# Kernel optimization log

Hardware: AMD Instinct MI355X
Metric: run time of the kernel (lower is better)

The kernel has to match this reference:

```python
import jax, jax.numpy as jnp
import numpy as np

N_EXPERTS = 6
TOP_K = 2
IN_DIM, HID_DIM, OUT_DIM = 1024, 4096, 1024
N_TOKENS = 8192


def setup_inputs() -> dict:
    key = jax.random.key(0)
    ks = jax.random.split(key, 7)
    s_in = 1.0 / np.sqrt(IN_DIM)
    s_hid = 1.0 / np.sqrt(HID_DIM)
    return {
        "x": jax.random.normal(ks[0], (N_TOKENS, IN_DIM), dtype=jnp.float32),
        "Wg": jax.random.uniform(ks[1], (IN_DIM, N_EXPERTS), jnp.float32, -s_in, s_in),
        "bg": jax.random.uniform(ks[2], (N_EXPERTS,), jnp.float32, -s_in, s_in),
        "W1": jax.random.uniform(ks[3], (N_EXPERTS, IN_DIM, HID_DIM), jnp.float32, -s_in, s_in),
        "b1": jax.random.uniform(ks[4], (N_EXPERTS, HID_DIM), jnp.float32, -s_in, s_in),
        "W2": jax.random.uniform(ks[5], (N_EXPERTS, HID_DIM, OUT_DIM), jnp.float32, -s_hid, s_hid),
        "b2": jax.random.uniform(ks[6], (N_EXPERTS, OUT_DIM), jnp.float32, -s_hid, s_hid),
    }


def reference(x, Wg, bg, W1, b1, W2, b2):
    n_experts = Wg.shape[-1]
    # gating: scores [N, E]
    scores = x @ Wg + bg
    _, topk_idx = jax.lax.top_k(scores, TOP_K)  # [N, k]
    # binary mask of selected experts [N, E]
    mask = jax.nn.one_hot(topk_idx, n_experts, dtype=scores.dtype).sum(axis=1)
    weights = jax.nn.softmax(scores, axis=-1) * mask
    weights = weights / (weights.sum(axis=-1, keepdims=True) + 1e-8)
    # dense all-expert compute (faithful to original): hidden [N, E, H]
    h = jax.nn.relu(jnp.einsum("ni,eih->neh", x, W1) + b1)
    outputs = jnp.einsum("neh,eho->neo", h, W2) + b2  # [N, E, O]
    return jnp.einsum("ne,neo->no", weights, outputs)
```

## Files before the change

### kernel.cpp

```cpp
#include <hip/hip_runtime.h>

typedef unsigned short u16;
typedef float f32x4 __attribute__((ext_vector_type(4)));
typedef __bf16 bf16x8 __attribute__((ext_vector_type(8)));
typedef unsigned short u16x8 __attribute__((ext_vector_type(8)));
typedef unsigned short u16x4 __attribute__((ext_vector_type(4)));

#define N_TOKENS 8192
#define IN_DIM   1024
#define HID_DIM  4096
#define OUT_DIM  1024
#define N_EXP    6

__device__ __forceinline__ u16 f2bf(float f) {
  union { float f; unsigned int u; } v; v.f = f;
  unsigned int u = v.u;
  unsigned int r = (u + 0x7FFFu + ((u >> 16) & 1u)) >> 16;
  return (u16)r;
}

__device__ __forceinline__ float bf2f(u16 v) {
  union { unsigned int u; float f; } x; x.u = ((unsigned int)v) << 16; return x.f;
}

__device__ __forceinline__ void load_lds16(const void* g, void* l) {
  __builtin_amdgcn_global_load_lds(
      (const __attribute__((address_space(1))) void*)g,
      (__attribute__((address_space(3))) void*)l, 16, 0, 0);
}

__global__ __launch_bounds__(256) void cvt_kernel(const float* __restrict__ src,
                                                  u16* __restrict__ dst, int n4) {
  int gid = blockIdx.x * 256 + threadIdx.x;
  int stride = gridDim.x * 256;
  for (int i = gid; i < n4; i += stride) {
    float4 v = ((const float4*)src)[i];
    u16x4 o; o[0] = f2bf(v.x); o[1] = f2bf(v.y); o[2] = f2bf(v.z); o[3] = f2bf(v.w);
    ((u16x4*)dst)[i] = o;
  }
}

__global__ __launch_bounds__(256) void transpose_cvt(const float* __restrict__ src,
                                                     u16* __restrict__ dst, int R, int C) {
  __shared__ u16 tile[64][72];
  const size_t esz = (size_t)R * C;
  src += (size_t)blockIdx.z * esz;
  dst += (size_t)blockIdx.z * esz;
  int c0 = blockIdx.x * 64, r0 = blockIdx.y * 64;
  int t = threadIdx.x;
  int cc = (t & 15) * 4, rb = t >> 4;
#pragma unroll
  for (int p = 0; p < 4; p++) {
    int r = p * 16 + rb;
    float4 v = *(const float4*)(src + (size_t)(r0 + r) * C + c0 + cc);
    tile[cc + 0][r] = f2bf(v.x);
    tile[cc + 1][r] = f2bf(v.y);
    tile[cc + 2][r] = f2bf(v.z);
    tile[cc + 3][r] = f2bf(v.w);
  }
  __syncthreads();
  int c = t >> 2, rp = (t & 3) * 16;
  u16* dp = dst + (size_t)(c0 + c) * R + r0 + rp;
  *(u16x8*)(dp)     = *(const u16x8*)&tile[c][rp];
  *(u16x8*)(dp + 8) = *(const u16x8*)&tile[c][rp + 8];
}

__global__ __launch_bounds__(256) void gating_kernel(const float* __restrict__ x,
                                                     const float* __restrict__ Wg,
                                                     const float* __restrict__ bg,
                                                     int* __restrict__ gate_e,
                                                     float* __restrict__ gate_w) {
  int lane = threadIdx.x & 63, wid = threadIdx.x >> 6;
  int tok = blockIdx.x * 4 + wid;
  float acc[N_EXP] = {0.f, 0.f, 0.f, 0.f, 0.f, 0.f};
  const float4* xr = (const float4*)(x + (size_t)tok * IN_DIM);
#pragma unroll
  for (int g = 0; g < 4; g++) {
    float4 v = xr[lane + g * 64];
    int c0 = (lane + g * 64) * 4;
#pragma unroll
    for (int c = 0; c < 4; c++) {
      float xv = (c == 0) ? v.x : (c == 1) ? v.y : (c == 2) ? v.z : v.w;
      const float* wr = Wg + (c0 + c) * N_EXP;
#pragma unroll
      for (int e = 0; e < N_EXP; e++) acc[e] += xv * wr[e];
    }
  }
#pragma unroll
  for (int e = 0; e < N_EXP; e++) {
    float a = acc[e];
#pragma unroll
    for (int off = 32; off > 0; off >>= 1) a += __shfl_xor(a, off, 64);
    acc[e] = a;
  }
  if (lane == 0) {
    float s[N_EXP];
#pragma unroll
    for (int e = 0; e < N_EXP; e++) s[e] = acc[e] + bg[e];
    float mx = s[0];
#pragma unroll
    for (int e = 1; e < N_EXP; e++) mx = fmaxf(mx, s[e]);
    float p[N_EXP], sum = 0.f;
#pragma unroll
    for (int e = 0; e < N_EXP; e++) { p[e] = expf(s[e] - mx); sum += p[e]; }
    int a = 0;
#pragma unroll
    for (int e = 1; e < N_EXP; e++) if (s[e] > s[a]) a = e;
    int b = (a == 0) ? 1 : 0;
#pragma unroll
    for (int e = 0; e < N_EXP; e++) if (e != a && s[e] > s[b]) b = e;
    float pa = p[a] / sum, pb = p[b] / sum;
    float den = pa + pb + 1e-8f;
    gate_e[2 * tok] = a; gate_e[2 * tok + 1] = b;
    gate_w[2 * tok] = pa / den; gate_w[2 * tok + 1] = pb / den;
  }
}

__global__ __launch_bounds__(384) void routing_kernel(const int* __restrict__ gate_e,
                                                      const float* __restrict__ gate_w,
                                                      int* __restrict__ idxl,
                                                      int* __restrict__ tokslot,
                                                      int* __restrict__ meta) {
  int wave = threadIdx.x >> 6, lane = threadIdx.x & 63;
  __shared__ int s_cnt[N_EXP];
  if (wave < N_EXP) {
    int e = wave, cnt = 0;
    for (int base = 0; base < N_TOKENS; base += 64) {
      int t = base + lane;
      int e0 = gate_e[2 * t], e1 = gate_e[2 * t + 1];
      bool sel = (e0 == e) || (e1 == e);
      unsigned long long m = __ballot(sel);
      int pos = __popcll(m & ((1ull << lane) - 1ull));
      if (sel) {
        int j = cnt + pos;
        idxl[e * N_TOKENS + j] = t;
        int k = (e0 == e) ? 0 : 1;
        tokslot[2 * t + k] = j;
      }
      cnt += __popcll(m);
    }
    if (lane == 0) s_cnt[e] = cnt;
  }
  __syncthreads();
  if (threadIdx.x == 0) {
    int off = 0;
    for (int e = 0; e < N_EXP; e++) { meta[e] = s_cnt[e]; meta[8 + e] = off; off += s_cnt[e]; }
    meta[8 + N_EXP] = off;
  }
}


#define GDS_A(AH) \
  _Pragma("unroll") for (int mi = 0; mi < 4; mi++) { \
    int r_ = (AH)*128 + wr*64 + mi*16 + lrow; \
    af[mi][0] = *(const bf16x8*)&sA[cur][r_*64 + ((lhi ^ lx7) * 8)]; \
    af[mi][1] = *(const bf16x8*)&sA[cur][r_*64 + (((4 + lhi) ^ lx7) * 8)]; }

#define GDS_B(BH) \
  _Pragma("unroll") for (int nj = 0; nj < 2; nj++) { \
    int r_ = (BH)*128 + wc*32 + nj*16 + lrow; \
    bfr[nj][0] = *(const bf16x8*)&sB[cur][r_*64 + ((lhi ^ lx7) * 8)]; \
    bfr[nj][1] = *(const bf16x8*)&sB[cur][r_*64 + (((4 + lhi) ^ lx7) * 8)]; }

#define GSTG_A(HH) \
  load_lds16(pa[HH][0] + ksn, &sA[nxt][((HH)*128 + wave*16) * 64]); \
  load_lds16(pa[HH][1] + ksn, &sA[nxt][((HH)*128 + wave*16 + 8) * 64]);

#define GSTG_B(HH) \
  load_lds16(pb[HH][0] + ksn, &sB[nxt][((HH)*128 + wave*16) * 64]); \
  load_lds16(pb[HH][1] + ksn, &sB[nxt][((HH)*128 + wave*16 + 8) * 64]);

#define GMFMA_Q(AH, BH) \
  _Pragma("unroll") for (int mi = 0; mi < 4; mi++) \
  _Pragma("unroll") for (int nj = 0; nj < 2; nj++) { \
    acc[AH][BH][mi][nj] = __builtin_amdgcn_mfma_f32_16x16x32_bf16(af[mi][0], bfr[nj][0], acc[AH][BH][mi][nj], 0, 0, 0); \
    acc[AH][BH][mi][nj] = __builtin_amdgcn_mfma_f32_16x16x32_bf16(af[mi][1], bfr[nj][1], acc[AH][BH][mi][nj], 0, 0, 0); }

#define GBAR __builtin_amdgcn_s_barrier()
#define GLGKM0 asm volatile("s_waitcnt lgkmcnt(0)" ::: "memory")
#define GVMC(n) asm volatile("s_waitcnt vmcnt(" #n ")" ::: "memory")

#define GEMM_KLOOP(NT_)                                                        \
  { const int ksn = 0; const int nxt = 0;                                      \
    GSTG_A(0); GSTG_B(0); GSTG_A(1); GSTG_B(1); }                              \
  GVMC(4);                                                                     \
  GBAR;                                                                        \
  int cur = 0;                                                                 \
  for (int t = 0; t < (NT_); t++) {                                            \
    const int nxt = cur ^ 1;                                                   \
    const int ksn = ((t + 1 < (NT_)) ? (t + 1) : ((NT_) - 1)) * 64;            \
                                                          \
    GDS_A(0); GDS_B(0);                                                        \
    GSTG_A(0);                                                                 \
    GBAR; GLGKM0;                                                              \
    __builtin_amdgcn_s_setprio(1); GMFMA_Q(0, 0); __builtin_amdgcn_s_setprio(0); \
    GVMC(2); GBAR;                                                             \
                                                          \
    GDS_B(1);                                                                  \
    GSTG_B(0);                                                                 \
    GBAR; GLGKM0;                                                              \
    __builtin_amdgcn_s_setprio(1); GMFMA_Q(0, 1); __builtin_amdgcn_s_setprio(0); \
    GBAR;                                                                      \
                                                          \
    GDS_A(1); GDS_B(0);                                                        \
    GSTG_A(1);                                                                 \
    GBAR; GLGKM0;                                                              \
    __builtin_amdgcn_s_setprio(1); GMFMA_Q(1, 0); __builtin_amdgcn_s_setprio(0); \
    GBAR;                                                                      \
                                                          \
    GDS_B(1);                                                                  \
    GSTG_B(1);                                                                 \
    GBAR; GLGKM0;                                                              \
    __builtin_amdgcn_s_setprio(1); GMFMA_Q(1, 1); __builtin_amdgcn_s_setprio(0); \
    GVMC(4); GBAR;                                                             \
    cur = nxt;                                                                 \
  }

__device__ __forceinline__ void decode_expert(const int* meta, int mtg,
                                              int& e, int& mt, int& cnt) {
  e = -1; mt = 0; cnt = 0;
  int sum = 0;
#pragma unroll
  for (int ee = 0; ee < N_EXP; ee++) {
    int c = meta[ee];
    int nt = (c + 255) >> 8;
    if (e < 0 && mtg < sum + nt) { e = ee; mt = mtg - sum; cnt = c; }
    sum += nt;
  }
}

__global__ __launch_bounds__(512) void gemm1_kernel(const u16* __restrict__ xb,
                                                    const u16* __restrict__ W1T,
                                                    const float* __restrict__ b1,
                                                    const int* __restrict__ idxl,
                                                    const int* __restrict__ meta,
                                                    u16* __restrict__ h) {
  __shared__ u16 sA[2][16384];
  __shared__ u16 sB[2][16384];
  const int bid = blockIdx.x;
  const int xcd = bid & 7;
  const int s = bid >> 3;
  const int chunk = s / 36, q = s % 36;
  const int n = chunk * 4 + (q & 3);
  const int mtg = xcd * 9 + (q >> 2);

  int e, mt, cnt;
  decode_expert(meta, mtg, e, mt, cnt);
  if (e < 0) return;
  const int off = meta[8 + e];
  const int bn0 = n * 256;
  const int tid = threadIdx.x, lane = tid & 63, wave = tid >> 6;
  const int wr = wave >> 2, wc = wave & 3;
  const int lrow = lane & 15, lhi = lane >> 4, lx7 = lane & 7;
  const int schunk = (lane & 7) ^ (lane >> 3);

  const u16* pa[2][2];
  const u16* pb[2][2];
  const u16* bbase = W1T + (size_t)e * HID_DIM * IN_DIM;
#pragma unroll
  for (int hh = 0; hh < 2; hh++)
#pragma unroll
    for (int i = 0; i < 2; i++) {
      int gr = hh * 128 + wave * 16 + i * 8 + (lane >> 3);
      int j = mt * 256 + gr; if (j >= cnt) j = cnt - 1;
      int tok = idxl[e * N_TOKENS + j];
      pa[hh][i] = xb + (size_t)tok * IN_DIM + schunk * 8;
      pb[hh][i] = bbase + (size_t)(bn0 + gr) * IN_DIM + schunk * 8;
    }

  f32x4 acc[2][2][4][2] = {};
  bf16x8 af[4][2], bfr[2][2];

  GEMM_KLOOP(IN_DIM / 64)

#pragma unroll
  for (int ah = 0; ah < 2; ah++)
#pragma unroll
    for (int bh = 0; bh < 2; bh++)
#pragma unroll
      for (int nj = 0; nj < 2; nj++) {
        int col = bn0 + bh * 128 + wc * 32 + nj * 16 + lrow;
        float bias = b1[e * HID_DIM + col];
#pragma unroll
        for (int mi = 0; mi < 4; mi++)
#pragma unroll
          for (int rr = 0; rr < 4; rr++) {
            int j = mt * 256 + ah * 128 + wr * 64 + mi * 16 + lhi * 4 + rr;
            if (j < cnt) {
              float v = fmaxf(acc[ah][bh][mi][nj][rr] + bias, 0.f);
              h[(size_t)(off + j) * HID_DIM + col] = f2bf(v);
            }
          }
      }
}

__global__ __launch_bounds__(512) void gemm2_kernel(const u16* __restrict__ hbuf,
                                                    const u16* __restrict__ W2T,
                                                    const float* __restrict__ b2,
                                                    const int* __restrict__ meta,
                                                    u16* __restrict__ y0,
                                                    u16* __restrict__ y1) {
  __shared__ u16 sA[2][16384];
  __shared__ u16 sB[2][16384];
  const int bid = blockIdx.x;
  const int xcd = bid & 7;
  const int s = bid >> 3;
  const int v = s & 7;
  const int mtg = xcd * 9 + (s >> 3);
  const int n = v >> 1, kzid = v & 1;

  int e, mt, cnt;
  decode_expert(meta, mtg, e, mt, cnt);
  if (e < 0) return;
  const int off = meta[8 + e];
  const int bn0 = n * 256;
  const int kz = kzid * (HID_DIM / 2);
  const int tid = threadIdx.x, lane = tid & 63, wave = tid >> 6;
  const int wr = wave >> 2, wc = wave & 3;
  const int lrow = lane & 15, lhi = lane >> 4, lx7 = lane & 7;
  const int schunk = (lane & 7) ^ (lane >> 3);

  const u16* pa[2][2];
  const u16* pb[2][2];
  const u16* bbase = W2T + (size_t)e * OUT_DIM * HID_DIM;
#pragma unroll
  for (int hh = 0; hh < 2; hh++)
#pragma unroll
    for (int i = 0; i < 2; i++) {
      int gr = hh * 128 + wave * 16 + i * 8 + (lane >> 3);
      int j = mt * 256 + gr; if (j >= cnt) j = cnt - 1;
      pa[hh][i] = hbuf + (size_t)(off + j) * HID_DIM + kz + schunk * 8;
      pb[hh][i] = bbase + (size_t)(bn0 + gr) * HID_DIM + kz + schunk * 8;
    }

  f32x4 acc[2][2][4][2] = {};
  bf16x8 af[4][2], bfr[2][2];

  GEMM_KLOOP(HID_DIM / 2 / 64)

  u16* __restrict__ yb = kzid ? y1 : y0;
#pragma unroll
  for (int ah = 0; ah < 2; ah++)
#pragma unroll
    for (int bh = 0; bh < 2; bh++)
#pragma unroll
      for (int nj = 0; nj < 2; nj++) {
        int col = bn0 + bh * 128 + wc * 32 + nj * 16 + lrow;
        float bias = (kzid == 0) ? b2[e * OUT_DIM + col] : 0.f;
#pragma unroll
        for (int mi = 0; mi < 4; mi++)
#pragma unroll
          for (int rr = 0; rr < 4; rr++) {
            int j = mt * 256 + ah * 128 + wr * 64 + mi * 16 + lhi * 4 + rr;
            if (j < cnt)
              yb[(size_t)(off + j) * OUT_DIM + col] = f2bf(acc[ah][bh][mi][nj][rr] + bias);
          }
      }
}

__global__ __launch_bounds__(256) void combine_kernel(const u16* __restrict__ y0,
                                                      const u16* __restrict__ y1,
                                                      const int* __restrict__ gate_e,
                                                      const float* __restrict__ gate_w,
                                                      const int* __restrict__ tokslot,
                                                      const int* __restrict__ meta,
                                                      float* __restrict__ out) {
  const int t = blockIdx.x;
  const int e0 = gate_e[2 * t], e1 = gate_e[2 * t + 1];
  const float w0 = gate_w[2 * t], w1 = gate_w[2 * t + 1];
  const size_t s0 = (size_t)(meta[8 + e0] + tokslot[2 * t]) * OUT_DIM;
  const size_t s1 = (size_t)(meta[8 + e1] + tokslot[2 * t + 1]) * OUT_DIM;
  const int c = threadIdx.x * 4;
  u16x4 a0 = *(const u16x4*)(y0 + s0 + c);
  u16x4 b0 = *(const u16x4*)(y1 + s0 + c);
  u16x4 a1 = *(const u16x4*)(y0 + s1 + c);
  u16x4 b1 = *(const u16x4*)(y1 + s1 + c);
  float4 o;
  o.x = w0 * (bf2f(a0[0]) + bf2f(b0[0])) + w1 * (bf2f(a1[0]) + bf2f(b1[0]));
  o.y = w0 * (bf2f(a0[1]) + bf2f(b0[1])) + w1 * (bf2f(a1[1]) + bf2f(b1[1]));
  o.z = w0 * (bf2f(a0[2]) + bf2f(b0[2])) + w1 * (bf2f(a1[2]) + bf2f(b1[2]));
  o.w = w0 * (bf2f(a0[3]) + bf2f(b0[3])) + w1 * (bf2f(a1[3]) + bf2f(b1[3]));
  *(float4*)(out + (size_t)t * OUT_DIM + c) = o;
}

extern "C" void kernel_launch(void* const* d_in, const int* in_sizes, int n_in,
                              void* d_out, int out_size, void* d_ws, size_t ws_size,
                              hipStream_t stream) {
  const float* x  = (const float*)d_in[0];
  const float* Wg = (const float*)d_in[1];
  const float* bg = (const float*)d_in[2];
  const float* W1 = (const float*)d_in[3];
  const float* b1 = (const float*)d_in[4];
  const float* W2 = (const float*)d_in[5];
  const float* b2 = (const float*)d_in[6];
  float* out = (float*)d_out;

  char* ws = (char*)d_ws;
  u16*   xb     = (u16*)(ws);
  u16*   W1T    = (u16*)(ws + 16777216);
  u16*   y0     = (u16*)(ws);
  u16*   y1     = (u16*)(ws + 33554432);
  u16*   W2T    = (u16*)(ws + 67108864);
  u16*   h      = (u16*)(ws + 117440512);
  int*   gate_e = (int*)(ws + 251658240);
  float* gate_w = (float*)(ws + 251723776);
  int*   idxl   = (int*)(ws + 251789312);
  int*   tokslot= (int*)(ws + 251985920);
  int*   meta   = (int*)(ws + 252051456);

  cvt_kernel<<<2048, 256, 0, stream>>>(x, xb, N_TOKENS * IN_DIM / 4);
  transpose_cvt<<<dim3(HID_DIM / 64, IN_DIM / 64, N_EXP), 256, 0, stream>>>(W1, W1T, IN_DIM, HID_DIM);
  transpose_cvt<<<dim3(OUT_DIM / 64, HID_DIM / 64, N_EXP), 256, 0, stream>>>(W2, W2T, HID_DIM, OUT_DIM);
  gating_kernel<<<2048, 256, 0, stream>>>(x, Wg, bg, gate_e, gate_w);
  routing_kernel<<<1, 384, 0, stream>>>(gate_e, gate_w, idxl, tokslot, meta);
  gemm1_kernel<<<1152, 512, 0, stream>>>(xb, W1T, b1, idxl, meta, h);
  gemm2_kernel<<<576, 512, 0, stream>>>(h, W2T, b2, meta, y0, y1);
  combine_kernel<<<N_TOKENS, 256, 0, stream>>>(y0, y1, gate_e, gate_w, tokslot, meta, out);
}
```

Measured before the change: 588.8 us.

## Fuse x bf16 conversion into gating and deepen GEMM k-loop prefetch pipeline

The standalone x-to-bf16 conversion kernel is removed, and the conversion is done inside the gating kernel, which already reads x. This saves one launch and one full pass over x. The GEMM k-loop is also restructured: it keeps two B register fragment sets and issues global-to-LDS loads for tile t+2 into the buffer just consumed, so more loads are in flight with a single vmcnt wait per iteration. The trade-off is extra register pressure and a more delicate buffer-reuse ordering across barriers.

```diff
diff --git a/kernel.cpp b/kernel.cpp
--- a/kernel.cpp
+++ b/kernel.cpp
@@ -27,17 +27,6 @@
   __builtin_amdgcn_global_load_lds(
       (const __attribute__((address_space(1))) void*)g,
       (__attribute__((address_space(3))) void*)l, 16, 0, 0);
-}
-
-__global__ __launch_bounds__(256) void cvt_kernel(const float* __restrict__ src,
-                                                  u16* __restrict__ dst, int n4) {
-  int gid = blockIdx.x * 256 + threadIdx.x;
-  int stride = gridDim.x * 256;
-  for (int i = gid; i < n4; i += stride) {
-    float4 v = ((const float4*)src)[i];
-    u16x4 o; o[0] = f2bf(v.x); o[1] = f2bf(v.y); o[2] = f2bf(v.z); o[3] = f2bf(v.w);
-    ((u16x4*)dst)[i] = o;
-  }
 }
 
 __global__ __launch_bounds__(256) void transpose_cvt(const float* __restrict__ src,
@@ -68,16 +57,20 @@
 __global__ __launch_bounds__(256) void gating_kernel(const float* __restrict__ x,
                                                      const float* __restrict__ Wg,
                                                      const float* __restrict__ bg,
+                                                     u16* __restrict__ xb,
                                                      int* __restrict__ gate_e,
                                                      float* __restrict__ gate_w) {
   int lane = threadIdx.x & 63, wid = threadIdx.x >> 6;
   int tok = blockIdx.x * 4 + wid;
   float acc[N_EXP] = {0.f, 0.f, 0.f, 0.f, 0.f, 0.f};
   const float4* xr = (const float4*)(x + (size_t)tok * IN_DIM);
+  u16* xw = xb + (size_t)tok * IN_DIM;
 #pragma unroll
   for (int g = 0; g < 4; g++) {
     float4 v = xr[lane + g * 64];
     int c0 = (lane + g * 64) * 4;
+    u16x4 o; o[0] = f2bf(v.x); o[1] = f2bf(v.y); o[2] = f2bf(v.z); o[3] = f2bf(v.w);
+    *(u16x4*)(xw + c0) = o;
 #pragma unroll
     for (int c = 0; c < 4; c++) {
       float xv = (c == 0) ? v.x : (c == 1) ? v.y : (c == 2) ? v.z : v.w;
@@ -156,64 +149,64 @@
     af[mi][0] = *(const bf16x8*)&sA[cur][r_*64 + ((lhi ^ lx7) * 8)]; \
     af[mi][1] = *(const bf16x8*)&sA[cur][r_*64 + (((4 + lhi) ^ lx7) * 8)]; }
 
-#define GDS_B(BH) \
+#define GDS_B(BH, R) \
   _Pragma("unroll") for (int nj = 0; nj < 2; nj++) { \
     int r_ = (BH)*128 + wc*32 + nj*16 + lrow; \
-    bfr[nj][0] = *(const bf16x8*)&sB[cur][r_*64 + ((lhi ^ lx7) * 8)]; \
-    bfr[nj][1] = *(const bf16x8*)&sB[cur][r_*64 + (((4 + lhi) ^ lx7) * 8)]; }
-
-#define GSTG_A(HH) \
-  load_lds16(pa[HH][0] + ksn, &sA[nxt][((HH)*128 + wave*16) * 64]); \
-  load_lds16(pa[HH][1] + ksn, &sA[nxt][((HH)*128 + wave*16 + 8) * 64]);
-
-#define GSTG_B(HH) \
-  load_lds16(pb[HH][0] + ksn, &sB[nxt][((HH)*128 + wave*16) * 64]); \
-  load_lds16(pb[HH][1] + ksn, &sB[nxt][((HH)*128 + wave*16 + 8) * 64]);
-
-#define GMFMA_Q(AH, BH) \
+    R[nj][0] = *(const bf16x8*)&sB[cur][r_*64 + ((lhi ^ lx7) * 8)]; \
+    R[nj][1] = *(const bf16x8*)&sB[cur][r_*64 + (((4 + lhi) ^ lx7) * 8)]; }
+
+#define STG_A(BUF, HH, KS) \
+  load_lds16(pa[HH][0] + (KS), &sA[BUF][((HH)*128 + wave*16) * 64]); \
+  load_lds16(pa[HH][1] + (KS), &sA[BUF][((HH)*128 + wave*16 + 8) * 64]);
+
+#define STG_B(BUF, HH, KS) \
+  load_lds16(pb[HH][0] + (KS), &sB[BUF][((HH)*128 + wave*16) * 64]); \
+  load_lds16(pb[HH][1] + (KS), &sB[BUF][((HH)*128 + wave*16 + 8) * 64]);
+
+#define GMFMA_Q(AH, BH, R) \
   _Pragma("unroll") for (int mi = 0; mi < 4; mi++) \
   _Pragma("unroll") for (int nj = 0; nj < 2; nj++) { \
-    acc[AH][BH][mi][nj] = __builtin_amdgcn_mfma_f32_16x16x32_bf16(af[mi][0], bfr[nj][0], acc[AH][BH][mi][nj], 0, 0, 0); \
-    acc[AH][BH][mi][nj] = __builtin_amdgcn_mfma_f32_16x16x32_bf16(af[mi][1], bfr[nj][1], acc[AH][BH][mi][nj], 0, 0, 0); }
+    acc[AH][BH][mi][nj] = __builtin_amdgcn_mfma_f32_16x16x32_bf16(af[mi][0], R[nj][0], acc[AH][BH][mi][nj], 0, 0, 0); \
+    acc[AH][BH][mi][nj] = __builtin_amdgcn_mfma_f32_16x16x32_bf16(af[mi][1], R[nj][1], acc[AH][BH][mi][nj], 0, 0, 0); }
 
 #define GBAR __builtin_amdgcn_s_barrier()
 #define GLGKM0 asm volatile("s_waitcnt lgkmcnt(0)" ::: "memory")
 #define GVMC(n) asm volatile("s_waitcnt vmcnt(" #n ")" ::: "memory")
+#define GPRIO1 __builtin_amdgcn_s_setprio(1)
+#define GPRIO0 __builtin_amdgcn_s_setprio(0)
 
 #define GEMM_KLOOP(NT_)                                                        \
-  { const int ksn = 0; const int nxt = 0;                                      \
-    GSTG_A(0); GSTG_B(0); GSTG_A(1); GSTG_B(1); }                              \
-  GVMC(4);                                                                     \
+                           \
+  { STG_A(0, 0, 0) STG_B(0, 0, 0) STG_A(0, 1, 0) STG_B(0, 1, 0)                \
+    STG_A(1, 0, 64) STG_B(1, 0, 64) STG_A(1, 1, 64) }                          \
+  GVMC(6);                                                                     \
   GBAR;                                                                        \
-  int cur = 0;                                                                 \
   for (int t = 0; t < (NT_); t++) {                                            \
-    const int nxt = cur ^ 1;                                                   \
-    const int ksn = ((t + 1 < (NT_)) ? (t + 1) : ((NT_) - 1)) * 64;            \
-                                                          \
-    GDS_A(0); GDS_B(0);                                                        \
-    GSTG_A(0);                                                                 \
+    const int cur = t & 1, nxt = cur ^ 1;                                      \
+    const int kB1 = ((t + 1 < (NT_)) ? (t + 1) : ((NT_) - 1)) * 64;            \
+    const int k2  = ((t + 2 < (NT_)) ? (t + 2) : ((NT_) - 1)) * 64;            \
+                             \
+    GDS_A(0); GDS_B(0, b0r);                                                   \
+    STG_B(nxt, 1, kB1)                                                         \
     GBAR; GLGKM0;                                                              \
-    __builtin_amdgcn_s_setprio(1); GMFMA_Q(0, 0); __builtin_amdgcn_s_setprio(0); \
-    GVMC(2); GBAR;                                                             \
-                                                          \
-    GDS_B(1);                                                                  \
-    GSTG_B(0);                                                                 \
+    GPRIO1; GMFMA_Q(0, 0, b0r); GPRIO0;                                        \
+    GBAR;                                                                      \
+                             \
+    GDS_B(1, b1r);                                                             \
+    STG_A(cur, 0, k2)                                                          \
     GBAR; GLGKM0;                                                              \
-    __builtin_amdgcn_s_setprio(1); GMFMA_Q(0, 1); __builtin_amdgcn_s_setprio(0); \
+    GPRIO1; GMFMA_Q(0, 1, b1r); GPRIO0;                                        \
     GBAR;                                                                      \
-                                                          \
-    GDS_A(1); GDS_B(0);                                                        \
-    GSTG_A(1);                                                                 \
+                             \
+    GDS_A(1);                                                                  \
+    STG_B(cur, 0, k2)                                                          \
     GBAR; GLGKM0;                                                              \
-    __builtin_amdgcn_s_setprio(1); GMFMA_Q(1, 0); __builtin_amdgcn_s_setprio(0); \
+    GPRIO1; GMFMA_Q(1, 0, b0r); GPRIO0;                                        \
     GBAR;                                                                      \
-                                                          \
-    GDS_B(1);                                                                  \
-    GSTG_B(1);                                                                 \
-    GBAR; GLGKM0;                                                              \
-    __builtin_amdgcn_s_setprio(1); GMFMA_Q(1, 1); __builtin_amdgcn_s_setprio(0); \
-    GVMC(4); GBAR;                                                             \
-    cur = nxt;                                                                 \
+        \
+    STG_A(cur, 1, k2)                                                          \
+    GPRIO1; GMFMA_Q(1, 1, b1r); GPRIO0;                                        \
+    GVMC(6); GBAR;                                                             \
   }
 
 __device__ __forceinline__ void decode_expert(const int* meta, int mtg,
@@ -269,7 +262,7 @@
     }
 
   f32x4 acc[2][2][4][2] = {};
-  bf16x8 af[4][2], bfr[2][2];
+  bf16x8 af[4][2], b0r[2][2], b1r[2][2];
 
   GEMM_KLOOP(IN_DIM / 64)
 
@@ -334,7 +327,7 @@
     }
 
   f32x4 acc[2][2][4][2] = {};
-  bf16x8 af[4][2], bfr[2][2];
+  bf16x8 af[4][2], b0r[2][2], b1r[2][2];
 
   GEMM_KLOOP(HID_DIM / 2 / 64)
 
@@ -408,10 +401,9 @@
   int*   tokslot= (int*)(ws + 251985920);
   int*   meta   = (int*)(ws + 252051456);
 
-  cvt_kernel<<<2048, 256, 0, stream>>>(x, xb, N_TOKENS * IN_DIM / 4);
   transpose_cvt<<<dim3(HID_DIM / 64, IN_DIM / 64, N_EXP), 256, 0, stream>>>(W1, W1T, IN_DIM, HID_DIM);
   transpose_cvt<<<dim3(OUT_DIM / 64, HID_DIM / 64, N_EXP), 256, 0, stream>>>(W2, W2T, HID_DIM, OUT_DIM);
-  gating_kernel<<<2048, 256, 0, stream>>>(x, Wg, bg, gate_e, gate_w);
+  gating_kernel<<<2048, 256, 0, stream>>>(x, Wg, bg, xb, gate_e, gate_w);
   routing_kernel<<<1, 384, 0, stream>>>(gate_e, gate_w, idxl, tokslot, meta);
   gemm1_kernel<<<1152, 512, 0, stream>>>(xb, W1T, b1, idxl, meta, h);
   gemm2_kernel<<<576, 512, 0, stream>>>(h, W2T, b2, meta, y0, y1);
```

After: 597.0 us. About the same (+1.4%).
